# Kernel tuning notes

Measured on AMD Instinct MI355X. Metric: run time of the kernel, lower is better.

## Reference

```python
import jax, jax.numpy as jnp
import numpy as np

B, L, D = 4, 4096, 1024  # batch, seq_len, d_model


def setup_inputs() -> dict:
    key = jax.random.key(0)
    k0, k1, k2 = jax.random.split(key, 3)
    x = jax.random.normal(k0, (B, L, D), dtype=jnp.float32)
    # Dense(d_model*3) applied to x: kernel [D, 3D], bias [3D]
    W_proj = jax.random.normal(k1, (D, 3 * D), dtype=jnp.float32) / np.sqrt(D)
    b_proj = jnp.zeros((3 * D,), dtype=jnp.float32)
    # Output Dense(d_model): kernel [D, D], bias [D]
    W_out = jax.random.normal(k2, (D, D), dtype=jnp.float32) / np.sqrt(D)
    b_out = jnp.zeros((D,), dtype=jnp.float32)
    return {"x": x, "W_proj": W_proj, "b_proj": b_proj,
            "W_out": W_out, "b_out": b_out,
            "layer_idx": 0, "num_layers": 12}


def reference(x, W_proj, b_proj, W_out, b_out, layer_idx, num_layers):
    # x: [B, L, D] -> x_proj: [B, L, 3D]
    x_proj = jnp.einsum('bld,de->ble', x, W_proj) + b_proj
    gate_input, forget_input, output_gate = jnp.split(x_proj, 3, axis=-1)
    # NOTE: in the source, forget_gate / input_gate / k / v / the lax.scan
    # recurrence are defined but never used to produce the output (dead code).
    # The live path is exactly:
    out = gate_input * jax.nn.sigmoid(output_gate)          # [B, L, D]
    out = jnp.einsum('bld,de->ble', out, W_out) + b_out     # [B, L, D]
    # Dropout is deterministic (training=False) -> identity.
    return out
```

## Files before the change

kernel.cpp:

```cpp
#include <hip/hip_runtime.h>
#include <hip/hip_bf16.h>


#define MTOT 16384
#define DM   1024
#define MEG  (1024 * 1024)

typedef __bf16 bf16x8 __attribute__((ext_vector_type(8)));
typedef float  f32x4  __attribute__((ext_vector_type(4)));

#define AS1 __attribute__((address_space(1)))
#define AS3 __attribute__((address_space(3)))

static __device__ __forceinline__ void async_load16(const void* g, void* l) {
    __builtin_amdgcn_global_load_lds((const AS1 void*)g, (AS3 void*)l, 16, 0, 0);
}

static __device__ __forceinline__ unsigned short f2bf(float f) {
    __hip_bfloat16 h = __float2bfloat16(f);
    return *(unsigned short*)&h;
}

__global__ __launch_bounds__(256)
void conv_x(const float* __restrict__ x, unsigned short* __restrict__ dst) {
    const size_t i = ((size_t)blockIdx.x * 256 + threadIdx.x) * 8;
    const f32x4 a = *(const f32x4*)(x + i);
    const f32x4 b = *(const f32x4*)(x + i + 4);
    __align__(16) unsigned short o[8];
    o[0] = f2bf(a[0]); o[1] = f2bf(a[1]); o[2] = f2bf(a[2]); o[3] = f2bf(a[3]);
    o[4] = f2bf(b[0]); o[5] = f2bf(b[1]); o[6] = f2bf(b[2]); o[7] = f2bf(b[3]);
    *(uint4*)(dst + i) = *(const uint4*)o;
}

__global__ void transpose_w(const float* __restrict__ Wproj, const float* __restrict__ Wout,
                            unsigned short* __restrict__ dst0) {
    __shared__ unsigned short t[32][33];
    const int z = blockIdx.z;
    const float* src;
    unsigned short* dst;
    int ld, coff;
    if (z == 0)      { src = Wproj; ld = 3072; coff = 0;    dst = dst0; }
    else if (z == 1) { src = Wproj; ld = 3072; coff = 2048; dst = dst0 + MEG; }
    else             { src = Wout;  ld = 1024; coff = 0;    dst = dst0 + 2 * MEG; }
    const int k0 = blockIdx.x * 32;
    const int n0 = blockIdx.y * 32;
    const int tx = threadIdx.x, ty = threadIdx.y;
    for (int i = ty; i < 32; i += 8)
        t[i][tx] = f2bf(src[(size_t)(k0 + i) * ld + coff + n0 + tx]);
    __syncthreads();
    for (int i = ty; i < 32; i += 8)
        dst[(size_t)(n0 + i) * DM + k0 + tx] = t[tx][i];
}

__global__ __launch_bounds__(256, 2)
void gemm1_fused(const unsigned short* __restrict__ X,
                 const unsigned short* __restrict__ WgT,
                 const unsigned short* __restrict__ WoT,
                 const float* __restrict__ bproj,
                 unsigned short* __restrict__ Hlo,
                 unsigned short* __restrict__ Hhi) {
    __shared__ __align__(16) unsigned short sA[128 * 32];
    __shared__ __align__(16) unsigned short sBg[64 * 32];
    __shared__ __align__(16) unsigned short sBo[64 * 32];

    const int tid  = threadIdx.x;
    const int wave = tid >> 6;
    const int lane = tid & 63;
    const int m0 = blockIdx.y * 128;
    const int n0 = blockIdx.x * 64;
    const int wm = (wave & 1) * 64;
    const int wn = (wave >> 1) * 32;

    unsigned short* __restrict__ H =
        (m0 < 8192) ? Hlo : (Hhi - (size_t)8192 * DM);

    f32x4 accG[4][2], accO[4][2];
#pragma unroll
    for (int i = 0; i < 4; ++i)
#pragma unroll
        for (int j = 0; j < 2; ++j) {
            accG[i][j] = (f32x4){0.f, 0.f, 0.f, 0.f};
            accO[i][j] = (f32x4){0.f, 0.f, 0.f, 0.f};
        }

    const int arow = tid >> 2;
    const int acol = (tid & 3) * 8;
    const int kq = (lane >> 4) * 8;
    const int rA = lane & 15;

    for (int k0 = 0; k0 < DM; k0 += 32) {
        async_load16(X + (size_t)(m0 + arow) * DM + k0 + acol,       (char*)sA + tid * 16);
        async_load16(X + (size_t)(m0 + 64 + arow) * DM + k0 + acol,  (char*)sA + 4096 + tid * 16);
        async_load16(WgT + (size_t)(n0 + arow) * DM + k0 + acol,     (char*)sBg + tid * 16);
        async_load16(WoT + (size_t)(n0 + arow) * DM + k0 + acol,     (char*)sBo + tid * 16);
        __syncthreads();

        bf16x8 af[4], bg[2], bo[2];
#pragma unroll
        for (int i = 0; i < 4; ++i)
            af[i] = *(const bf16x8*)&sA[(wm + i * 16 + rA) * 32 + kq];
#pragma unroll
        for (int j = 0; j < 2; ++j) {
            bg[j] = *(const bf16x8*)&sBg[(wn + j * 16 + rA) * 32 + kq];
            bo[j] = *(const bf16x8*)&sBo[(wn + j * 16 + rA) * 32 + kq];
        }
#pragma unroll
        for (int i = 0; i < 4; ++i)
#pragma unroll
            for (int j = 0; j < 2; ++j) {
                accG[i][j] = __builtin_amdgcn_mfma_f32_16x16x32_bf16(af[i], bg[j], accG[i][j], 0, 0, 0);
                accO[i][j] = __builtin_amdgcn_mfma_f32_16x16x32_bf16(af[i], bo[j], accO[i][j], 0, 0, 0);
            }
        __syncthreads();
    }

    const int colL = lane & 15;
    const int rowQ = (lane >> 4) * 4;
#pragma unroll
    for (int j = 0; j < 2; ++j) {
        const int n = n0 + wn + j * 16 + colL;
        const float bgv = bproj[n];
        const float bov = bproj[2048 + n];
#pragma unroll
        for (int i = 0; i < 4; ++i) {
            const int mbase = m0 + wm + i * 16 + rowQ;
#pragma unroll
            for (int r = 0; r < 4; ++r) {
                const float g = accG[i][j][r] + bgv;
                const float o = accO[i][j][r] + bov;
                const float h = g * (1.0f / (1.0f + __expf(-o)));
                H[(size_t)(mbase + r) * DM + n] = f2bf(h);
            }
        }
    }
}

__global__ __launch_bounds__(256, 2)
void gemm2(const unsigned short* __restrict__ Hlo,
           const unsigned short* __restrict__ Hhi,
           const unsigned short* __restrict__ Bt,
           const float* __restrict__ bout,
           float* __restrict__ Out,
           int row_base) {
    __shared__ __align__(16) unsigned short sA[128 * 32];
    __shared__ __align__(16) unsigned short sB[128 * 32];

    const int tid  = threadIdx.x;
    const int wave = tid >> 6;
    const int lane = tid & 63;
    const int m0 = row_base + blockIdx.y * 128;
    const int n0 = blockIdx.x * 128;
    const int wm = (wave & 1) * 64;
    const int wn = (wave >> 1) * 64;

    const unsigned short* __restrict__ A =
        (m0 < 8192) ? (Hlo + (size_t)m0 * DM) : (Hhi + (size_t)(m0 - 8192) * DM);

    f32x4 acc[4][4];
#pragma unroll
    for (int i = 0; i < 4; ++i)
#pragma unroll
        for (int j = 0; j < 4; ++j) acc[i][j] = (f32x4){0.f, 0.f, 0.f, 0.f};

    const int arow = tid >> 2;
    const int acol = (tid & 3) * 8;
    const int kq = (lane >> 4) * 8;
    const int rA = lane & 15;

    for (int k0 = 0; k0 < DM; k0 += 32) {
        async_load16(A + (size_t)arow * DM + k0 + acol,        (char*)sA + tid * 16);
        async_load16(A + (size_t)(64 + arow) * DM + k0 + acol, (char*)sA + 4096 + tid * 16);
        async_load16(Bt + (size_t)(n0 + arow) * DM + k0 + acol,      (char*)sB + tid * 16);
        async_load16(Bt + (size_t)(n0 + 64 + arow) * DM + k0 + acol, (char*)sB + 4096 + tid * 16);
        __syncthreads();

        bf16x8 af[4], bfr[4];
#pragma unroll
        for (int i = 0; i < 4; ++i)
            af[i] = *(const bf16x8*)&sA[(wm + i * 16 + rA) * 32 + kq];
#pragma unroll
        for (int j = 0; j < 4; ++j)
            bfr[j] = *(const bf16x8*)&sB[(wn + j * 16 + rA) * 32 + kq];
#pragma unroll
        for (int i = 0; i < 4; ++i)
#pragma unroll
            for (int j = 0; j < 4; ++j)
                acc[i][j] = __builtin_amdgcn_mfma_f32_16x16x32_bf16(af[i], bfr[j], acc[i][j], 0, 0, 0);
        __syncthreads();
    }

    const int colL = lane & 15;
    const int rowQ = (lane >> 4) * 4;
#pragma unroll
    for (int j = 0; j < 4; ++j) {
        const int n = n0 + wn + j * 16 + colL;
        const float bv = bout[n];
#pragma unroll
        for (int i = 0; i < 4; ++i) {
            const int mbase = m0 + wm + i * 16 + rowQ;
#pragma unroll
            for (int r = 0; r < 4; ++r)
                Out[(size_t)(mbase + r) * DM + n] = acc[i][j][r] + bv;
        }
    }
}

extern "C" void kernel_launch(void* const* d_in, const int* in_sizes, int n_in,
                              void* d_out, int out_size, void* d_ws, size_t ws_size,
                              hipStream_t stream) {
    const float* x     = (const float*)d_in[0];
    const float* Wproj = (const float*)d_in[1];
    const float* bproj = (const float*)d_in[2];
    const float* Wout  = (const float*)d_in[3];
    const float* bout  = (const float*)d_in[4];
    float* out = (float*)d_out;

    unsigned short* Xb  = (unsigned short*)d_out;
    unsigned short* WgT   = (unsigned short*)d_ws;
    unsigned short* WoT   = WgT + MEG;
    unsigned short* WoutT = WgT + 2 * MEG;
    unsigned short* Hws   = WgT + 3 * MEG;

    const bool big_ws = ws_size >= (size_t)19 * MEG * 2;

    unsigned short* Hlo = big_ws ? Hws : ((unsigned short*)d_out + 16 * MEG);
    unsigned short* Hhi = big_ws ? (Hws + (size_t)8192 * DM) : Hws;

    conv_x<<<(MTOT * DM) / (256 * 8), 256, 0, stream>>>(x, Xb);

    transpose_w<<<dim3(32, 32, 3), dim3(32, 8, 1), 0, stream>>>(Wproj, Wout, WgT);

    gemm1_fused<<<dim3(DM / 64, MTOT / 128), 256, 0, stream>>>(
        Xb, WgT, WoT, bproj, Hlo, Hhi);

    if (big_ws) {
        gemm2<<<dim3(DM / 128, MTOT / 128), 256, 0, stream>>>(
            Hlo, Hhi, WoutT, bout, out, 0);
    } else {
        gemm2<<<dim3(DM / 128, 64), 256, 0, stream>>>(Hlo, Hhi, WoutT, bout, out, 0);
        gemm2<<<dim3(DM / 128, 64), 256, 0, stream>>>(Hlo, Hhi, WoutT, bout, out, 8192);
    }
}
```

Measured before the change: 268.1 us.

## Rewrite both GEMMs with 256x256 double-buffered LDS tiles and phased pipelining

Both GEMM kernels move to 512-thread blocks with 256-row tiles and a K step of 64. LDS is double-buffered with an XOR swizzle, and async global-to-LDS loads for upcoming K tiles are interleaved across four barrier-separated MFMA phases, with s_setprio raised around the MFMA bursts. Block IDs are swizzled for L2 locality. The aim is to raise arithmetic intensity and hide global memory latency behind MFMA work, at the cost of large LDS use (128 KB per block), one block per CU, and intricate hand-written vmcnt/barrier bookkeeping that is easy to get wrong.

```diff
diff --git a/kernel.cpp b/kernel.cpp
--- a/kernel.cpp
+++ b/kernel.cpp
@@ -52,156 +52,298 @@
         dst[(size_t)(n0 + i) * DM + k0 + tx] = t[tx][i];
 }
 
-__global__ __launch_bounds__(256, 2)
+__global__ __launch_bounds__(512)
 void gemm1_fused(const unsigned short* __restrict__ X,
                  const unsigned short* __restrict__ WgT,
                  const unsigned short* __restrict__ WoT,
                  const float* __restrict__ bproj,
                  unsigned short* __restrict__ Hlo,
                  unsigned short* __restrict__ Hhi) {
-    __shared__ __align__(16) unsigned short sA[128 * 32];
-    __shared__ __align__(16) unsigned short sBg[64 * 32];
-    __shared__ __align__(16) unsigned short sBo[64 * 32];
+    __shared__ __align__(16) unsigned short sA[2][256 * 64];
+    __shared__ __align__(16) unsigned short sB[2][256 * 64];
 
     const int tid  = threadIdx.x;
     const int wave = tid >> 6;
     const int lane = tid & 63;
-    const int m0 = blockIdx.y * 128;
-    const int n0 = blockIdx.x * 64;
-    const int wm = (wave & 1) * 64;
-    const int wn = (wave >> 1) * 32;
+    const int wm = wave & 1;
+    const int wn = wave >> 1;
+
+    const int bid = blockIdx.x;
+    const int swz = (bid & 7) * 64 + (bid >> 3);
+    const int m0 = (swz >> 3) * 256;
+    const int n0 = (swz & 7) * 128;
 
     unsigned short* __restrict__ H =
         (m0 < 8192) ? Hlo : (Hhi - (size_t)8192 * DM);
 
-    f32x4 accG[4][2], accO[4][2];
-#pragma unroll
-    for (int i = 0; i < 4; ++i)
-#pragma unroll
-        for (int j = 0; j < 2; ++j) {
-            accG[i][j] = (f32x4){0.f, 0.f, 0.f, 0.f};
-            accO[i][j] = (f32x4){0.f, 0.f, 0.f, 0.f};
-        }
-
-    const int arow = tid >> 2;
-    const int acol = (tid & 3) * 8;
-    const int kq = (lane >> 4) * 8;
     const int rA = lane & 15;
-
-    for (int k0 = 0; k0 < DM; k0 += 32) {
-        async_load16(X + (size_t)(m0 + arow) * DM + k0 + acol,       (char*)sA + tid * 16);
-        async_load16(X + (size_t)(m0 + 64 + arow) * DM + k0 + acol,  (char*)sA + 4096 + tid * 16);
-        async_load16(WgT + (size_t)(n0 + arow) * DM + k0 + acol,     (char*)sBg + tid * 16);
-        async_load16(WoT + (size_t)(n0 + arow) * DM + k0 + acol,     (char*)sBo + tid * 16);
-        __syncthreads();
-
-        bf16x8 af[4], bg[2], bo[2];
-#pragma unroll
-        for (int i = 0; i < 4; ++i)
-            af[i] = *(const bf16x8*)&sA[(wm + i * 16 + rA) * 32 + kq];
-#pragma unroll
-        for (int j = 0; j < 2; ++j) {
-            bg[j] = *(const bf16x8*)&sBg[(wn + j * 16 + rA) * 32 + kq];
-            bo[j] = *(const bf16x8*)&sBo[(wn + j * 16 + rA) * 32 + kq];
-        }
-#pragma unroll
-        for (int i = 0; i < 4; ++i)
-#pragma unroll
-            for (int j = 0; j < 2; ++j) {
-                accG[i][j] = __builtin_amdgcn_mfma_f32_16x16x32_bf16(af[i], bg[j], accG[i][j], 0, 0, 0);
-                accO[i][j] = __builtin_amdgcn_mfma_f32_16x16x32_bf16(af[i], bo[j], accO[i][j], 0, 0, 0);
+    const int qq = lane >> 4;
+    const int r7 = rA & 7;
+    const int swq   = ((qq ^ (r7 & 3)) << 4);
+    const int k0off = ((rA >> 2) & 1) << 6;
+    const int k1off = k0off ^ 64;
+    const int ldsA_base = (wm * 64 + rA) * 128 + swq;
+    const int ldsB_base = (wn * 16 + rA) * 128 + swq;
+
+    const int trow = tid >> 3;
+    const int tsw  = (((tid & 7) ^ (trow & 7)) << 4);
+    const char* srcA  = (const char*)X   + (size_t)(m0 + trow) * 2048 + tsw;
+    const char* srcBg = (const char*)WgT + (size_t)(n0 + trow) * 2048 + tsw;
+    const char* srcBo = (const char*)WoT + (size_t)(n0 + trow) * 2048 + tsw;
+    char* dA = (char*)&sA[0][0] + tid * 16;
+    char* dB = (char*)&sB[0][0] + tid * 16;
+
+#define STA1(b, kt, r)  async_load16(srcA  + (kt) * 128 + (r) * 131072, dA + (b) * 32768 + (r) * 8192)
+#define STBG1(b, kt, r) async_load16(srcBg + (kt) * 128 + (r) * 131072, dB + (b) * 32768 + (r) * 8192)
+#define STBO1(b, kt, r) async_load16(srcBo + (kt) * 128 + (r) * 131072, dB + (b) * 32768 + (2 + (r)) * 8192)
+#define LDA1(dst, bb, h, il, kof) dst = *(const bf16x8*)((const char*)sA + (bb) * 32768 + ldsA_base + (h) * 16384 + (il) * 2048 + (kof))
+#define LDB1(dst, bb, mat, j, kof) dst = *(const bf16x8*)((const char*)sB + (bb) * 32768 + ldsB_base + (mat) * 16384 + (j) * 8192 + (kof))
+
+    f32x4 aG[2][4][2], aO[2][4][2];
+    bf16x8 fa[4][2], fbg[2], fbo[2];
+
+    STA1(0, 0, 0); STA1(0, 0, 1); STA1(0, 0, 2); STA1(0, 0, 3);
+    STBG1(0, 0, 0); STBG1(0, 0, 1); STBO1(0, 0, 0); STBO1(0, 0, 1);
+    STBG1(1, 1, 0); STBO1(1, 1, 0); STA1(1, 1, 2); STA1(1, 1, 3);
+
+#pragma unroll
+    for (int h = 0; h < 2; ++h)
+#pragma unroll
+        for (int il = 0; il < 4; ++il)
+#pragma unroll
+            for (int jl = 0; jl < 2; ++jl) {
+                aG[h][il][jl] = (f32x4){0.f, 0.f, 0.f, 0.f};
+                aO[h][il][jl] = (f32x4){0.f, 0.f, 0.f, 0.f};
             }
-        __syncthreads();
-    }
+
+    asm volatile("s_waitcnt vmcnt(4)" ::: "memory");
+    __builtin_amdgcn_s_barrier();
+
+#define MM1(H_, JL) do { \
+    _Pragma("unroll") \
+    for (int il = 0; il < 4; ++il) { \
+        aG[H_][il][JL] = __builtin_amdgcn_mfma_f32_16x16x32_bf16(fa[il][0], fbg[0], aG[H_][il][JL], 0, 0, 0); \
+        aO[H_][il][JL] = __builtin_amdgcn_mfma_f32_16x16x32_bf16(fa[il][0], fbo[0], aO[H_][il][JL], 0, 0, 0); \
+        aG[H_][il][JL] = __builtin_amdgcn_mfma_f32_16x16x32_bf16(fa[il][1], fbg[1], aG[H_][il][JL], 0, 0, 0); \
+        aO[H_][il][JL] = __builtin_amdgcn_mfma_f32_16x16x32_bf16(fa[il][1], fbo[1], aO[H_][il][JL], 0, 0, 0); \
+    } } while (0)
+
+#define PHASE_SYNC() \
+    __builtin_amdgcn_s_barrier(); \
+    asm volatile("s_waitcnt lgkmcnt(0)" ::: "memory"); \
+    __builtin_amdgcn_sched_barrier(0)
+
+#define TILE1(kt, b, nb) do { \
+     \
+    _Pragma("unroll") \
+    for (int il = 0; il < 4; ++il) { LDA1(fa[il][0], b, 0, il, k0off); LDA1(fa[il][1], b, 0, il, k1off); } \
+    LDB1(fbg[0], b, 0, 0, k0off); LDB1(fbg[1], b, 0, 0, k1off); \
+    LDB1(fbo[0], b, 1, 0, k0off); LDB1(fbo[1], b, 1, 0, k1off); \
+    if ((kt) < 15) { STA1(nb, (kt) + 1, 0); STBG1(nb, (kt) + 1, 1); } \
+    PHASE_SYNC(); \
+    __builtin_amdgcn_s_setprio(1); MM1(0, 0); __builtin_amdgcn_s_setprio(0); \
+    __builtin_amdgcn_s_barrier(); \
+     \
+    _Pragma("unroll") \
+    for (int il = 0; il < 4; ++il) { LDA1(fa[il][0], b, 1, il, k0off); LDA1(fa[il][1], b, 1, il, k1off); } \
+    if ((kt) < 15) { STA1(nb, (kt) + 1, 1); STBO1(nb, (kt) + 1, 1); } \
+    PHASE_SYNC(); \
+    __builtin_amdgcn_s_setprio(1); MM1(1, 0); __builtin_amdgcn_s_setprio(0); \
+    __builtin_amdgcn_s_barrier(); \
+     \
+    LDB1(fbg[0], b, 0, 1, k0off); LDB1(fbg[1], b, 0, 1, k1off); \
+    LDB1(fbo[0], b, 1, 1, k0off); LDB1(fbo[1], b, 1, 1, k1off); \
+    if ((kt) < 14) { STBG1(b, (kt) + 2, 0); STBO1(b, (kt) + 2, 0); } \
+    PHASE_SYNC(); \
+    __builtin_amdgcn_s_setprio(1); MM1(1, 1); __builtin_amdgcn_s_setprio(0); \
+    __builtin_amdgcn_s_barrier(); \
+     \
+    _Pragma("unroll") \
+    for (int il = 0; il < 4; ++il) { LDA1(fa[il][0], b, 0, il, k0off); LDA1(fa[il][1], b, 0, il, k1off); } \
+    if ((kt) < 14) { STA1(b, (kt) + 2, 2); STA1(b, (kt) + 2, 3); } \
+    PHASE_SYNC(); \
+    __builtin_amdgcn_s_setprio(1); MM1(0, 1); __builtin_amdgcn_s_setprio(0); \
+    if ((kt) < 14) { asm volatile("s_waitcnt vmcnt(4)" ::: "memory"); } \
+    else           { asm volatile("s_waitcnt vmcnt(0)" ::: "memory"); } \
+    __builtin_amdgcn_s_barrier(); \
+} while (0)
+
+#pragma unroll 1
+    for (int kt2 = 0; kt2 < 16; kt2 += 2) {
+        TILE1(kt2, 0, 1);
+        TILE1(kt2 + 1, 1, 0);
+    }
+#undef TILE1
+#undef MM1
+#undef STA1
+#undef STBG1
+#undef STBO1
+#undef LDA1
+#undef LDB1
 
     const int colL = lane & 15;
     const int rowQ = (lane >> 4) * 4;
 #pragma unroll
-    for (int j = 0; j < 2; ++j) {
-        const int n = n0 + wn + j * 16 + colL;
+    for (int jl = 0; jl < 2; ++jl) {
+        const int n = n0 + wn * 16 + jl * 64 + colL;
         const float bgv = bproj[n];
         const float bov = bproj[2048 + n];
 #pragma unroll
-        for (int i = 0; i < 4; ++i) {
-            const int mbase = m0 + wm + i * 16 + rowQ;
-#pragma unroll
-            for (int r = 0; r < 4; ++r) {
-                const float g = accG[i][j][r] + bgv;
-                const float o = accO[i][j][r] + bov;
-                const float h = g * (1.0f / (1.0f + __expf(-o)));
-                H[(size_t)(mbase + r) * DM + n] = f2bf(h);
+        for (int h = 0; h < 2; ++h)
+#pragma unroll
+            for (int il = 0; il < 4; ++il) {
+                const int mbase = m0 + wm * 64 + h * 128 + il * 16 + rowQ;
+#pragma unroll
+                for (int r = 0; r < 4; ++r) {
+                    const float g = aG[h][il][jl][r] + bgv;
+                    const float o = aO[h][il][jl][r] + bov;
+                    const float hv = g * (1.0f / (1.0f + __expf(-o)));
+                    H[(size_t)(mbase + r) * DM + n] = f2bf(hv);
+                }
             }
-        }
-    }
-}
-
-__global__ __launch_bounds__(256, 2)
+    }
+}
+
+__global__ __launch_bounds__(512)
 void gemm2(const unsigned short* __restrict__ Hlo,
            const unsigned short* __restrict__ Hhi,
            const unsigned short* __restrict__ Bt,
            const float* __restrict__ bout,
            float* __restrict__ Out,
            int row_base) {
-    __shared__ __align__(16) unsigned short sA[128 * 32];
-    __shared__ __align__(16) unsigned short sB[128 * 32];
+    __shared__ __align__(16) unsigned short sA[2][256 * 64];
+    __shared__ __align__(16) unsigned short sB[2][256 * 64];
 
     const int tid  = threadIdx.x;
     const int wave = tid >> 6;
     const int lane = tid & 63;
-    const int m0 = row_base + blockIdx.y * 128;
-    const int n0 = blockIdx.x * 128;
-    const int wm = (wave & 1) * 64;
-    const int wn = (wave >> 1) * 64;
+    const int wm = wave & 1;
+    const int wn = wave >> 1;
+
+    const int bid = blockIdx.x;
+    const int q8  = (int)gridDim.x >> 3;
+    const int swz = (bid & 7) * q8 + (bid >> 3);
+    const int m0 = row_base + (swz >> 2) * 256;
+    const int n0 = (swz & 3) * 256;
 
     const unsigned short* __restrict__ A =
         (m0 < 8192) ? (Hlo + (size_t)m0 * DM) : (Hhi + (size_t)(m0 - 8192) * DM);
 
-    f32x4 acc[4][4];
-#pragma unroll
-    for (int i = 0; i < 4; ++i)
-#pragma unroll
-        for (int j = 0; j < 4; ++j) acc[i][j] = (f32x4){0.f, 0.f, 0.f, 0.f};
-
-    const int arow = tid >> 2;
-    const int acol = (tid & 3) * 8;
-    const int kq = (lane >> 4) * 8;
     const int rA = lane & 15;
-
-    for (int k0 = 0; k0 < DM; k0 += 32) {
-        async_load16(A + (size_t)arow * DM + k0 + acol,        (char*)sA + tid * 16);
-        async_load16(A + (size_t)(64 + arow) * DM + k0 + acol, (char*)sA + 4096 + tid * 16);
-        async_load16(Bt + (size_t)(n0 + arow) * DM + k0 + acol,      (char*)sB + tid * 16);
-        async_load16(Bt + (size_t)(n0 + 64 + arow) * DM + k0 + acol, (char*)sB + 4096 + tid * 16);
-        __syncthreads();
-
-        bf16x8 af[4], bfr[4];
-#pragma unroll
-        for (int i = 0; i < 4; ++i)
-            af[i] = *(const bf16x8*)&sA[(wm + i * 16 + rA) * 32 + kq];
-#pragma unroll
-        for (int j = 0; j < 4; ++j)
-            bfr[j] = *(const bf16x8*)&sB[(wn + j * 16 + rA) * 32 + kq];
-#pragma unroll
-        for (int i = 0; i < 4; ++i)
+    const int qq = lane >> 4;
+    const int r7 = rA & 7;
+    const int swq   = ((qq ^ (r7 & 3)) << 4);
+    const int k0off = ((rA >> 2) & 1) << 6;
+    const int k1off = k0off ^ 64;
+    const int ldsA_base = (wm * 64 + rA) * 128 + swq;
+    const int ldsB_base = (wn * 16 + rA) * 128 + swq;
+
+    const int trow = tid >> 3;
+    const int tsw  = (((tid & 7) ^ (trow & 7)) << 4);
+    const char* srcA = (const char*)A  + (size_t)trow * 2048 + tsw;
+    const char* srcB = (const char*)Bt + (size_t)(n0 + trow) * 2048 + tsw;
+    char* dA = (char*)&sA[0][0] + tid * 16;
+    char* dB = (char*)&sB[0][0] + tid * 16;
+
+#define STA2(b, kt, r) async_load16(srcA + (kt) * 128 + (r) * 131072, dA + (b) * 32768 + (r) * 8192)
+#define STB2(b, kt, r) async_load16(srcB + (kt) * 128 + (r) * 131072, dB + (b) * 32768 + (r) * 8192)
+#define LDA2(dst, bb, h, il, kof) dst = *(const bf16x8*)((const char*)sA + (bb) * 32768 + ldsA_base + (h) * 16384 + (il) * 2048 + (kof))
+#define LDB2(dst, bb, j, kof)     dst = *(const bf16x8*)((const char*)sB + (bb) * 32768 + ldsB_base + (j) * 8192 + (kof))
+
+    f32x4 acc[2][4][4];
+    bf16x8 fa[4][2], fb[2][2];
+
+    STA2(0, 0, 0); STA2(0, 0, 1); STA2(0, 0, 2); STA2(0, 0, 3);
+    STB2(0, 0, 0); STB2(0, 0, 1); STB2(0, 0, 2); STB2(0, 0, 3);
+    STB2(1, 1, 0); STB2(1, 1, 1); STA2(1, 1, 2); STA2(1, 1, 3);
+
+#pragma unroll
+    for (int h = 0; h < 2; ++h)
+#pragma unroll
+        for (int il = 0; il < 4; ++il)
 #pragma unroll
             for (int j = 0; j < 4; ++j)
-                acc[i][j] = __builtin_amdgcn_mfma_f32_16x16x32_bf16(af[i], bfr[j], acc[i][j], 0, 0, 0);
-        __syncthreads();
-    }
+                acc[h][il][j] = (f32x4){0.f, 0.f, 0.f, 0.f};
+
+    asm volatile("s_waitcnt vmcnt(4)" ::: "memory");
+    __builtin_amdgcn_s_barrier();
+
+#define MM2(H_, JB) do { \
+    _Pragma("unroll") \
+    for (int il = 0; il < 4; ++il) { \
+        acc[H_][il][JB]     = __builtin_amdgcn_mfma_f32_16x16x32_bf16(fa[il][0], fb[0][0], acc[H_][il][JB], 0, 0, 0); \
+        acc[H_][il][JB + 1] = __builtin_amdgcn_mfma_f32_16x16x32_bf16(fa[il][0], fb[1][0], acc[H_][il][JB + 1], 0, 0, 0); \
+        acc[H_][il][JB]     = __builtin_amdgcn_mfma_f32_16x16x32_bf16(fa[il][1], fb[0][1], acc[H_][il][JB], 0, 0, 0); \
+        acc[H_][il][JB + 1] = __builtin_amdgcn_mfma_f32_16x16x32_bf16(fa[il][1], fb[1][1], acc[H_][il][JB + 1], 0, 0, 0); \
+    } } while (0)
+
+#define PHASE_SYNC2() \
+    __builtin_amdgcn_s_barrier(); \
+    asm volatile("s_waitcnt lgkmcnt(0)" ::: "memory"); \
+    __builtin_amdgcn_sched_barrier(0)
+
+#define TILE2(kt, b, nb) do { \
+     \
+    _Pragma("unroll") \
+    for (int il = 0; il < 4; ++il) { LDA2(fa[il][0], b, 0, il, k0off); LDA2(fa[il][1], b, 0, il, k1off); } \
+    LDB2(fb[0][0], b, 0, k0off); LDB2(fb[0][1], b, 0, k1off); \
+    LDB2(fb[1][0], b, 1, k0off); LDB2(fb[1][1], b, 1, k1off); \
+    if ((kt) < 15) { STA2(nb, (kt) + 1, 0); STB2(nb, (kt) + 1, 2); } \
+    PHASE_SYNC2(); \
+    __builtin_amdgcn_s_setprio(1); MM2(0, 0); __builtin_amdgcn_s_setprio(0); \
+    __builtin_amdgcn_s_barrier(); \
+     \
+    _Pragma("unroll") \
+    for (int il = 0; il < 4; ++il) { LDA2(fa[il][0], b, 1, il, k0off); LDA2(fa[il][1], b, 1, il, k1off); } \
+    if ((kt) < 15) { STA2(nb, (kt) + 1, 1); STB2(nb, (kt) + 1, 3); } \
+    PHASE_SYNC2(); \
+    __builtin_amdgcn_s_setprio(1); MM2(1, 0); __builtin_amdgcn_s_setprio(0); \
+    __builtin_amdgcn_s_barrier(); \
+     \
+    LDB2(fb[0][0], b, 2, k0off); LDB2(fb[0][1], b, 2, k1off); \
+    LDB2(fb[1][0], b, 3, k0off); LDB2(fb[1][1], b, 3, k1off); \
+    if ((kt) < 14) { STB2(b, (kt) + 2, 0); STB2(b, (kt) + 2, 1); } \
+    PHASE_SYNC2(); \
+    __builtin_amdgcn_s_setprio(1); MM2(1, 2); __builtin_amdgcn_s_setprio(0); \
+    __builtin_amdgcn_s_barrier(); \
+     \
+    _Pragma("unroll") \
+    for (int il = 0; il < 4; ++il) { LDA2(fa[il][0], b, 0, il, k0off); LDA2(fa[il][1], b, 0, il, k1off); } \
+    if ((kt) < 14) { STA2(b, (kt) + 2, 2); STA2(b, (kt) + 2, 3); } \
+    PHASE_SYNC2(); \
+    __builtin_amdgcn_s_setprio(1); MM2(0, 2); __builtin_amdgcn_s_setprio(0); \
+    if ((kt) < 14) { asm volatile("s_waitcnt vmcnt(4)" ::: "memory"); } \
+    else           { asm volatile("s_waitcnt vmcnt(0)" ::: "memory"); } \
+    __builtin_amdgcn_s_barrier(); \
+} while (0)
+
+#pragma unroll 1
+    for (int kt2 = 0; kt2 < 16; kt2 += 2) {
+        TILE2(kt2, 0, 1);
+        TILE2(kt2 + 1, 1, 0);
+    }
+#undef TILE2
+#undef MM2
+#undef STA2
+#undef STB2
+#undef LDA2
+#undef LDB2
 
     const int colL = lane & 15;
     const int rowQ = (lane >> 4) * 4;
 #pragma unroll
     for (int j = 0; j < 4; ++j) {
-        const int n = n0 + wn + j * 16 + colL;
+        const int n = n0 + wn * 16 + j * 64 + colL;
         const float bv = bout[n];
 #pragma unroll
-        for (int i = 0; i < 4; ++i) {
-            const int mbase = m0 + wm + i * 16 + rowQ;
-#pragma unroll
-            for (int r = 0; r < 4; ++r)
-                Out[(size_t)(mbase + r) * DM + n] = acc[i][j][r] + bv;
-        }
+        for (int h = 0; h < 2; ++h)
+#pragma unroll
+            for (int il = 0; il < 4; ++il) {
+                const int mbase = m0 + wm * 64 + h * 128 + il * 16 + rowQ;
+#pragma unroll
+                for (int r = 0; r < 4; ++r)
+                    Out[(size_t)(mbase + r) * DM + n] = acc[h][il][j][r] + bv;
+            }
     }
 }
 
@@ -230,14 +372,12 @@
 
     transpose_w<<<dim3(32, 32, 3), dim3(32, 8, 1), 0, stream>>>(Wproj, Wout, WgT);
 
-    gemm1_fused<<<dim3(DM / 64, MTOT / 128), 256, 0, stream>>>(
-        Xb, WgT, WoT, bproj, Hlo, Hhi);
+    gemm1_fused<<<512, 512, 0, stream>>>(Xb, WgT, WoT, bproj, Hlo, Hhi);
 
     if (big_ws) {
-        gemm2<<<dim3(DM / 128, MTOT / 128), 256, 0, stream>>>(
-            Hlo, Hhi, WoutT, bout, out, 0);
+        gemm2<<<256, 512, 0, stream>>>(Hlo, Hhi, WoutT, bout, out, 0);
     } else {
-        gemm2<<<dim3(DM / 128, 64), 256, 0, stream>>>(Hlo, Hhi, WoutT, bout, out, 0);
-        gemm2<<<dim3(DM / 128, 64), 256, 0, stream>>>(Hlo, Hhi, WoutT, bout, out, 8192);
-    }
-}
+        gemm2<<<128, 512, 0, stream>>>(Hlo, Hhi, WoutT, bout, out, 0);
+        gemm2<<<128, 512, 0, stream>>>(Hlo, Hhi, WoutT, bout, out, 8192);
+    }
+}
```

Measured after the change: 244.1 us. 9.0% less time.

## Replace LDS-staged GEMM tiles with direct global fragment loads and swizzled 256x128 blocks

Applied to the files above, without the earlier changes.

Both GEMM kernels stop staging A/B tiles through shared memory with async global-to-LDS loads and barriers. Each wave now reads its MFMA fragments directly from global memory. Blocks grow to 512 threads covering 256x128 output tiles, and a 1-D grid with a block-index swizzle is meant to improve L2 locality. This removes LDS traffic and synchronization, at the cost of uncoalesced strided loads, redundant fragment reads across waves, and no software prefetch.

```diff
diff --git a/kernel.cpp b/kernel.cpp
--- a/kernel.cpp
+++ b/kernel.cpp
@@ -8,13 +8,6 @@
 
 typedef __bf16 bf16x8 __attribute__((ext_vector_type(8)));
 typedef float  f32x4  __attribute__((ext_vector_type(4)));
-
-#define AS1 __attribute__((address_space(1)))
-#define AS3 __attribute__((address_space(3)))
-
-static __device__ __forceinline__ void async_load16(const void* g, void* l) {
-    __builtin_amdgcn_global_load_lds((const AS1 void*)g, (AS3 void*)l, 16, 0, 0);
-}
 
 static __device__ __forceinline__ unsigned short f2bf(float f) {
     __hip_bfloat16 h = __float2bfloat16(f);
@@ -52,155 +45,156 @@
         dst[(size_t)(n0 + i) * DM + k0 + tx] = t[tx][i];
 }
 
-__global__ __launch_bounds__(256, 2)
+__global__ __launch_bounds__(512)
 void gemm1_fused(const unsigned short* __restrict__ X,
                  const unsigned short* __restrict__ WgT,
                  const unsigned short* __restrict__ WoT,
                  const float* __restrict__ bproj,
                  unsigned short* __restrict__ Hlo,
                  unsigned short* __restrict__ Hhi) {
-    __shared__ __align__(16) unsigned short sA[128 * 32];
-    __shared__ __align__(16) unsigned short sBg[64 * 32];
-    __shared__ __align__(16) unsigned short sBo[64 * 32];
-
     const int tid  = threadIdx.x;
     const int wave = tid >> 6;
     const int lane = tid & 63;
-    const int m0 = blockIdx.y * 128;
-    const int n0 = blockIdx.x * 64;
-    const int wm = (wave & 1) * 64;
-    const int wn = (wave >> 1) * 32;
+    const int wm = wave & 1;
+    const int wn = wave >> 1;
+
+    const int bid = blockIdx.x;
+    const int swz = (bid & 7) * 64 + (bid >> 3);
+    const int m0 = (swz >> 3) * 256;
+    const int n0 = (swz & 7) * 128;
 
     unsigned short* __restrict__ H =
         (m0 < 8192) ? Hlo : (Hhi - (size_t)8192 * DM);
 
-    f32x4 accG[4][2], accO[4][2];
-#pragma unroll
-    for (int i = 0; i < 4; ++i)
-#pragma unroll
-        for (int j = 0; j < 2; ++j) {
-            accG[i][j] = (f32x4){0.f, 0.f, 0.f, 0.f};
-            accO[i][j] = (f32x4){0.f, 0.f, 0.f, 0.f};
+    const int rA = lane & 15;
+    const int kq = (lane >> 4) * 8;
+
+    const char* pA  = (const char*)X   + ((size_t)(m0 + wm * 64 + rA) * DM + kq) * 2;
+    const char* pBg = (const char*)WgT + ((size_t)(n0 + wn * 16 + rA) * DM + kq) * 2;
+    const char* pBo = (const char*)WoT + ((size_t)(n0 + wn * 16 + rA) * DM + kq) * 2;
+
+    f32x4 aG[2][4][2], aO[2][4][2];
+#pragma unroll
+    for (int h = 0; h < 2; ++h)
+#pragma unroll
+        for (int il = 0; il < 4; ++il)
+#pragma unroll
+            for (int jl = 0; jl < 2; ++jl) {
+                aG[h][il][jl] = (f32x4){0.f, 0.f, 0.f, 0.f};
+                aO[h][il][jl] = (f32x4){0.f, 0.f, 0.f, 0.f};
+            }
+
+#pragma unroll 1
+    for (int kt = 0; kt < 32; ++kt) {
+        const int kb = kt * 64;
+        bf16x8 fa[2][4], fbg[2], fbo[2];
+#pragma unroll
+        for (int h = 0; h < 2; ++h)
+#pragma unroll
+            for (int il = 0; il < 4; ++il)
+                fa[h][il] = *(const bf16x8*)(pA + (size_t)(h * 128 + il * 16) * 2048 + kb);
+#pragma unroll
+        for (int jl = 0; jl < 2; ++jl) {
+            fbg[jl] = *(const bf16x8*)(pBg + (size_t)(jl * 64) * 2048 + kb);
+            fbo[jl] = *(const bf16x8*)(pBo + (size_t)(jl * 64) * 2048 + kb);
         }
-
-    const int arow = tid >> 2;
-    const int acol = (tid & 3) * 8;
-    const int kq = (lane >> 4) * 8;
-    const int rA = lane & 15;
-
-    for (int k0 = 0; k0 < DM; k0 += 32) {
-        async_load16(X + (size_t)(m0 + arow) * DM + k0 + acol,       (char*)sA + tid * 16);
-        async_load16(X + (size_t)(m0 + 64 + arow) * DM + k0 + acol,  (char*)sA + 4096 + tid * 16);
-        async_load16(WgT + (size_t)(n0 + arow) * DM + k0 + acol,     (char*)sBg + tid * 16);
-        async_load16(WoT + (size_t)(n0 + arow) * DM + k0 + acol,     (char*)sBo + tid * 16);
-        __syncthreads();
-
-        bf16x8 af[4], bg[2], bo[2];
-#pragma unroll
-        for (int i = 0; i < 4; ++i)
-            af[i] = *(const bf16x8*)&sA[(wm + i * 16 + rA) * 32 + kq];
-#pragma unroll
-        for (int j = 0; j < 2; ++j) {
-            bg[j] = *(const bf16x8*)&sBg[(wn + j * 16 + rA) * 32 + kq];
-            bo[j] = *(const bf16x8*)&sBo[(wn + j * 16 + rA) * 32 + kq];
-        }
-#pragma unroll
-        for (int i = 0; i < 4; ++i)
-#pragma unroll
-            for (int j = 0; j < 2; ++j) {
-                accG[i][j] = __builtin_amdgcn_mfma_f32_16x16x32_bf16(af[i], bg[j], accG[i][j], 0, 0, 0);
-                accO[i][j] = __builtin_amdgcn_mfma_f32_16x16x32_bf16(af[i], bo[j], accO[i][j], 0, 0, 0);
-            }
-        __syncthreads();
+#pragma unroll
+        for (int h = 0; h < 2; ++h)
+#pragma unroll
+            for (int il = 0; il < 4; ++il)
+#pragma unroll
+                for (int jl = 0; jl < 2; ++jl) {
+                    aG[h][il][jl] = __builtin_amdgcn_mfma_f32_16x16x32_bf16(fa[h][il], fbg[jl], aG[h][il][jl], 0, 0, 0);
+                    aO[h][il][jl] = __builtin_amdgcn_mfma_f32_16x16x32_bf16(fa[h][il], fbo[jl], aO[h][il][jl], 0, 0, 0);
+                }
     }
 
     const int colL = lane & 15;
     const int rowQ = (lane >> 4) * 4;
 #pragma unroll
-    for (int j = 0; j < 2; ++j) {
-        const int n = n0 + wn + j * 16 + colL;
+    for (int jl = 0; jl < 2; ++jl) {
+        const int n = n0 + wn * 16 + jl * 64 + colL;
         const float bgv = bproj[n];
         const float bov = bproj[2048 + n];
 #pragma unroll
-        for (int i = 0; i < 4; ++i) {
-            const int mbase = m0 + wm + i * 16 + rowQ;
-#pragma unroll
-            for (int r = 0; r < 4; ++r) {
-                const float g = accG[i][j][r] + bgv;
-                const float o = accO[i][j][r] + bov;
-                const float h = g * (1.0f / (1.0f + __expf(-o)));
-                H[(size_t)(mbase + r) * DM + n] = f2bf(h);
+        for (int h = 0; h < 2; ++h)
+#pragma unroll
+            for (int il = 0; il < 4; ++il) {
+                const int mbase = m0 + wm * 64 + h * 128 + il * 16 + rowQ;
+#pragma unroll
+                for (int r = 0; r < 4; ++r) {
+                    const float g = aG[h][il][jl][r] + bgv;
+                    const float o = aO[h][il][jl][r] + bov;
+                    const float hv = g * (1.0f / (1.0f + __expf(-o)));
+                    H[(size_t)(mbase + r) * DM + n] = f2bf(hv);
+                }
             }
-        }
-    }
-}
-
-__global__ __launch_bounds__(256, 2)
+    }
+}
+
+__global__ __launch_bounds__(512)
 void gemm2(const unsigned short* __restrict__ Hlo,
            const unsigned short* __restrict__ Hhi,
            const unsigned short* __restrict__ Bt,
            const float* __restrict__ bout,
            float* __restrict__ Out,
            int row_base) {
-    __shared__ __align__(16) unsigned short sA[128 * 32];
-    __shared__ __align__(16) unsigned short sB[128 * 32];
-
     const int tid  = threadIdx.x;
     const int wave = tid >> 6;
     const int lane = tid & 63;
-    const int m0 = row_base + blockIdx.y * 128;
-    const int n0 = blockIdx.x * 128;
-    const int wm = (wave & 1) * 64;
-    const int wn = (wave >> 1) * 64;
+    const int wm = wave & 3;
+    const int wn = wave >> 2;
+
+    const int bid = blockIdx.x;
+    const int q8  = (int)gridDim.x >> 3;
+    const int swz = (bid & 7) * q8 + (bid >> 3);
+    const int m0 = row_base + (swz >> 3) * 256;
+    const int n0 = (swz & 7) * 128;
 
     const unsigned short* __restrict__ A =
         (m0 < 8192) ? (Hlo + (size_t)m0 * DM) : (Hhi + (size_t)(m0 - 8192) * DM);
 
+    const int rA = lane & 15;
+    const int kq = (lane >> 4) * 8;
+
+    const char* pA = (const char*)A  + ((size_t)(wm * 64 + rA) * DM + kq) * 2;
+    const char* pB = (const char*)Bt + ((size_t)(n0 + wn * 64 + rA) * DM + kq) * 2;
+
     f32x4 acc[4][4];
 #pragma unroll
-    for (int i = 0; i < 4; ++i)
-#pragma unroll
-        for (int j = 0; j < 4; ++j) acc[i][j] = (f32x4){0.f, 0.f, 0.f, 0.f};
-
-    const int arow = tid >> 2;
-    const int acol = (tid & 3) * 8;
-    const int kq = (lane >> 4) * 8;
-    const int rA = lane & 15;
-
-    for (int k0 = 0; k0 < DM; k0 += 32) {
-        async_load16(A + (size_t)arow * DM + k0 + acol,        (char*)sA + tid * 16);
-        async_load16(A + (size_t)(64 + arow) * DM + k0 + acol, (char*)sA + 4096 + tid * 16);
-        async_load16(Bt + (size_t)(n0 + arow) * DM + k0 + acol,      (char*)sB + tid * 16);
-        async_load16(Bt + (size_t)(n0 + 64 + arow) * DM + k0 + acol, (char*)sB + 4096 + tid * 16);
-        __syncthreads();
-
-        bf16x8 af[4], bfr[4];
-#pragma unroll
-        for (int i = 0; i < 4; ++i)
-            af[i] = *(const bf16x8*)&sA[(wm + i * 16 + rA) * 32 + kq];
-#pragma unroll
-        for (int j = 0; j < 4; ++j)
-            bfr[j] = *(const bf16x8*)&sB[(wn + j * 16 + rA) * 32 + kq];
-#pragma unroll
-        for (int i = 0; i < 4; ++i)
-#pragma unroll
-            for (int j = 0; j < 4; ++j)
-                acc[i][j] = __builtin_amdgcn_mfma_f32_16x16x32_bf16(af[i], bfr[j], acc[i][j], 0, 0, 0);
-        __syncthreads();
+    for (int il = 0; il < 4; ++il)
+#pragma unroll
+        for (int j = 0; j < 4; ++j) acc[il][j] = (f32x4){0.f, 0.f, 0.f, 0.f};
+
+#pragma unroll 1
+    for (int kt = 0; kt < 32; ++kt) {
+        const int kb = kt * 64;
+        bf16x8 fa[4], fb[4];
+#pragma unroll
+        for (int il = 0; il < 4; ++il)
+            fa[il] = *(const bf16x8*)(pA + (size_t)(il * 16) * 2048 + kb);
+#pragma unroll
+        for (int jl = 0; jl < 4; ++jl)
+            fb[jl] = *(const bf16x8*)(pB + (size_t)(jl * 16) * 2048 + kb);
+#pragma unroll
+        for (int il = 0; il < 4; ++il)
+#pragma unroll
+            for (int jl = 0; jl < 4; ++jl)
+                acc[il][jl] = __builtin_amdgcn_mfma_f32_16x16x32_bf16(fa[il], fb[jl], acc[il][jl], 0, 0, 0);
     }
 
     const int colL = lane & 15;
     const int rowQ = (lane >> 4) * 4;
 #pragma unroll
-    for (int j = 0; j < 4; ++j) {
-        const int n = n0 + wn + j * 16 + colL;
+    for (int jl = 0; jl < 4; ++jl) {
+        const int n = n0 + wn * 64 + jl * 16 + colL;
         const float bv = bout[n];
 #pragma unroll
-        for (int i = 0; i < 4; ++i) {
-            const int mbase = m0 + wm + i * 16 + rowQ;
+        for (int il = 0; il < 4; ++il) {
+            const int mbase = m0 + wm * 64 + il * 16 + rowQ;
 #pragma unroll
             for (int r = 0; r < 4; ++r)
-                Out[(size_t)(mbase + r) * DM + n] = acc[i][j][r] + bv;
+                Out[(size_t)(mbase + r) * DM + n] = acc[il][jl][r] + bv;
         }
     }
 }
@@ -230,14 +224,12 @@
 
     transpose_w<<<dim3(32, 32, 3), dim3(32, 8, 1), 0, stream>>>(Wproj, Wout, WgT);
 
-    gemm1_fused<<<dim3(DM / 64, MTOT / 128), 256, 0, stream>>>(
-        Xb, WgT, WoT, bproj, Hlo, Hhi);
+    gemm1_fused<<<512, 512, 0, stream>>>(Xb, WgT, WoT, bproj, Hlo, Hhi);
 
     if (big_ws) {
-        gemm2<<<dim3(DM / 128, MTOT / 128), 256, 0, stream>>>(
-            Hlo, Hhi, WoutT, bout, out, 0);
+        gemm2<<<512, 512, 0, stream>>>(Hlo, Hhi, WoutT, bout, out, 0);
     } else {
-        gemm2<<<dim3(DM / 128, 64), 256, 0, stream>>>(Hlo, Hhi, WoutT, bout, out, 0);
-        gemm2<<<dim3(DM / 128, 64), 256, 0, stream>>>(Hlo, Hhi, WoutT, bout, out, 8192);
-    }
-}
+        gemm2<<<256, 512, 0, stream>>>(Hlo, Hhi, WoutT, bout, out, 0);
+        gemm2<<<256, 512, 0, stream>>>(Hlo, Hhi, WoutT, bout, out, 8192);
+    }
+}
```

New measurement: 430.8 us. +60.7%, slower.
